# Optimization experiments

Hardware: AMD Instinct MI355X
Metric: run time of the kernel (lower is better)

Reference implementation:

```python
import jax, jax.numpy as jnp
import numpy as np

PATCH = 4   # patch_size
TOPK = 2    # top_k

B, H, W, C = 4, 128, 128, 256
FF, E = 1024, 4


def setup_inputs() -> dict:
    key = jax.random.key(0)
    k1, k2, k3, k4 = jax.random.split(key, 4)
    x = jax.random.normal(k1, (B, H, W, C), dtype=jnp.float32)
    Wg = jax.random.normal(k2, (E, C), dtype=jnp.float32) * 0.01   # router gate (std=0.01 init)
    lim1 = (6.0 / (C + FF)) ** 0.5                                  # xavier_uniform bounds
    W1 = jax.random.uniform(k3, (E, FF, C), minval=-lim1, maxval=lim1, dtype=jnp.float32)
    b1 = jnp.zeros((E, FF), dtype=jnp.float32)
    W2 = jax.random.uniform(k4, (E, C, FF), minval=-lim1, maxval=lim1, dtype=jnp.float32)
    b2 = jnp.zeros((E, C), dtype=jnp.float32)
    return {"x": x, "Wg": Wg, "W1": W1, "b1": b1, "W2": W2, "b2": b2}


def reference(x, Wg, W1, b1, W2, b2):
    Bs, Hs, Ws, Cs = x.shape
    Es = Wg.shape[0]
    ph = pw = PATCH
    nh, nw = Hs // ph, Ws // pw
    P = nh * nw
    # [B, nh, ph, nw, pw, C]
    xp = x.reshape(Bs, nh, ph, nw, pw, Cs)
    # --- router: per-patch avg pool + linear gate ---
    means = xp.mean(axis=(2, 4))                                  # [B, nh, nw, C]
    logits = jnp.einsum('bhwc,ec->bhwe', means, Wg).reshape(Bs, P, Es)
    probs = jax.nn.softmax(logits, axis=-1)
    w, idx = jax.lax.top_k(probs, TOPK)                           # [B, P, K]
    w = w / (w.sum(axis=-1, keepdims=True) + 1e-9)
    # dense combine weights per expert: [B, P, E]
    comb = (jax.nn.one_hot(idx, Es, dtype=w.dtype) * w[..., None]).sum(axis=-2)
    # --- expert dispatch/combine over patch tokens ---
    tokens = xp.transpose(0, 1, 3, 2, 4, 5).reshape(Bs, P, ph * pw, Cs)  # [B,P,T,C]
    out = jnp.zeros_like(tokens)
    for e in range(Es):  # small fixed expert set
        h = jax.nn.gelu(jnp.einsum('bptc,fc->bptf', tokens, W1[e]) + b1[e],
                        approximate=False)
        y = jnp.einsum('bptf,cf->bptc', h, W2[e]) + b2[e]
        out = out + comb[:, :, e, None, None] * y
    # reassemble patches -> [B, H, W, C]
    out = out.reshape(Bs, nh, nw, ph, pw, Cs).transpose(0, 1, 3, 2, 4, 5)
    return out.reshape(Bs, Hs, Ws, Cs)
```

## Files before the change

### kernel.cpp

```cpp
#include <hip/hip_runtime.h>
#include <hip/hip_bf16.h>
#include <cstdint>

#define NB 4
#define NH 128
#define NW 128
#define NC 256
#define NFF 1024
#define NE 4
#define NPATCH 4096
#define NPAIR 16
#define PPB 4
#define BM 64
#define FFC 128
#define NCHUNK_TOT 16

typedef __attribute__((ext_vector_type(8))) short short8;
typedef __attribute__((ext_vector_type(8))) unsigned short ushort8;
typedef __attribute__((ext_vector_type(4))) float f32x4;

__device__ __forceinline__ unsigned short f2b(float f) {
  union { float f; uint32_t u; } v; v.f = f;
  uint32_t u = v.u + 0x7FFFu + ((v.u >> 16) & 1u);
  return (unsigned short)(u >> 16);
}

__device__ __forceinline__ float gelu_f(float v) {
  float u = v * v;
  float t = __builtin_fmaf(u, 0.044715f, 1.0f) * v;
  float e = __builtin_amdgcn_exp2f(t * -2.3022083f);
  return v * __builtin_amdgcn_rcpf(1.0f + e);
}

__device__ __forceinline__ void bar_lgkm() {
  asm volatile("s_waitcnt lgkmcnt(0)" ::: "memory");
  __builtin_amdgcn_s_barrier();
}

__global__ __launch_bounds__(256) void convert_kernel(
    const float* __restrict__ W1, const float* __restrict__ W2,
    unsigned short* __restrict__ W1b, unsigned short* __restrict__ W2b,
    int* __restrict__ cnt, int n) {
  int i = blockIdx.x * blockDim.x + threadIdx.x;
  if (i < NPAIR) cnt[i] = 0;
  if (i < n) {
    W1b[i] = f2b(W1[i]);
    W2b[i] = f2b(W2[i]);
  }
}

__global__ __launch_bounds__(256) void router_kernel(
    const float* __restrict__ x, const float* __restrict__ Wg,
    int* __restrict__ cnt, int* __restrict__ plist, float2* __restrict__ wlist) {
  int p = blockIdx.x;
  int b = p >> 10, pi = p & 1023;
  int phi = pi >> 5, pwi = pi & 31;
  int c = threadIdx.x;

  const float* base = x + (((size_t)(b * NH + phi * 4) * NW) + pwi * 4) * NC + c;
  float s = 0.f;
#pragma unroll
  for (int i = 0; i < 4; i++)
#pragma unroll
    for (int j = 0; j < 4; j++)
      s += base[(i * NW + j) * NC];
  float mean = s * (1.f / 16.f);

  __shared__ float m_lds[NC];
  __shared__ double logit_lds[NE];
  m_lds[c] = mean;
  __syncthreads();

  int wid = c >> 6, lane = c & 63;
  {
    const float* wg = Wg + wid * NC;
    double acc = 0.0;
#pragma unroll
    for (int q = 0; q < 4; q++)
      acc += (double)m_lds[lane + q * 64] * (double)wg[lane + q * 64];
    for (int off = 32; off; off >>= 1) acc += __shfl_down(acc, off);
    if (lane == 0) logit_lds[wid] = acc;
  }
  __syncthreads();

  if (c == 0) {
    double l[NE], pp[NE];
    double mx = -1e300;
#pragma unroll
    for (int i = 0; i < NE; i++) { l[i] = logit_lds[i]; mx = fmax(mx, l[i]); }
    double sum = 0.0;
#pragma unroll
    for (int i = 0; i < NE; i++) { pp[i] = exp(l[i] - mx); sum += pp[i]; }
#pragma unroll
    for (int i = 0; i < NE; i++) pp[i] /= sum;
    int i1 = 0; double p1 = pp[0];
    for (int i = 1; i < NE; i++) if (pp[i] > p1) { p1 = pp[i]; i1 = i; }
    int i2 = -1; double p2 = -1.0;
    for (int i = 0; i < NE; i++) {
      if (i == i1) continue;
      if (pp[i] > p2) { p2 = pp[i]; i2 = i; }
    }
    double den = p1 + p2 + 1e-9;
    float w1 = (float)(p1 / den), w2 = (float)(p2 / den);
    int pr = i1 * NE + i2;
    int pos = atomicAdd(&cnt[pr], 1);
    plist[pr * NPATCH + pos] = p;
    wlist[pr * NPATCH + pos] = make_float2(w1, w2);
  }
}

__global__ __launch_bounds__(64) void worklist_kernel(
    const int* __restrict__ cnt, int* __restrict__ wl) {
  int lane = threadIdx.x;
  int cA[8], cB[8], mx = 0;
#pragma unroll
  for (int xc = 0; xc < 8; ++xc) {
    cA[xc] = (cnt[xc] + PPB - 1) / PPB;
    cB[xc] = (cnt[xc + 8] + PPB - 1) / PPB;
    int t = cA[xc] + cB[xc];
    mx = (t > mx) ? t : mx;
  }
  if (lane == 0) wl[0] = 8 * mx;
  int x = lane & 7, sub = lane >> 3;
  int nA = cA[x], tot = cA[x] + cB[x];
  for (int r = sub; r < mx; r += 8) {
    int ent = -1;
    if (r < nA) ent = (x << 12) | (r * PPB);
    else if (r < tot) ent = ((x + 8) << 12) | ((r - nA) * PPB);
    wl[1 + x + 8 * r] = ent;
  }
}

__global__ __launch_bounds__(512, 4) void ffn_kernel(
    const float* __restrict__ x, const float* __restrict__ b1,
    const float* __restrict__ b2, const unsigned short* __restrict__ W1b,
    const unsigned short* __restrict__ W2b, const int* __restrict__ cnt,
    const int* __restrict__ plist, const float2* __restrict__ wlist,
    const int* __restrict__ wl, float* __restrict__ out) {
  __shared__ unsigned short Xl[BM * NC];
  __shared__ unsigned short Hl[2][BM * FFC];

  int slot = blockIdx.x;
  if (slot >= wl[0]) return;
  int ent = wl[1 + slot];
  if (ent < 0) return;
  int pr = ent >> 12, pbase = ent & 4095;
  int e1 = pr >> 2, e2 = pr & 3;
  int n = cnt[pr];

  int tid = threadIdx.x, lane = tid & 63, wid = tid >> 6;
  int l15 = lane & 15;
  int kgrp = (lane >> 4) * 8;

  const int*    pl  = plist + pr * NPATCH + pbase;
  const float2* wlp = wlist + pr * NPATCH + pbase;

  float wvA[PPB], wvB[PPB];
#pragma unroll
  for (int q = 0; q < PPB; q++) {
    if (pbase + q < n) { float2 w = wlp[q]; wvA[q] = w.x; wvB[q] = w.y; }
    else { wvA[q] = 0.f; wvB[q] = 0.f; }
  }

  {
    int r  = tid >> 3;
    int c0 = (tid & 7) * 32;
    int pid = (pbase + (r >> 4) < n) ? pl[r >> 4] : -1;
    int t = r & 15;
    if (pid >= 0) {
      int b = pid >> 10, pi = pid & 1023;
      int phi = pi >> 5, pwi = pi & 31;
      const float* src =
          x + (((size_t)(b * NH + phi * 4 + (t >> 2)) * NW) + pwi * 4 + (t & 3)) * NC + c0;
#pragma unroll
      for (int q = 0; q < 4; q++) {
        float4 v0 = *reinterpret_cast<const float4*>(src + q * 8);
        float4 v1 = *reinterpret_cast<const float4*>(src + q * 8 + 4);
        ushort8 h;
        h[0] = f2b(v0.x); h[1] = f2b(v0.y); h[2] = f2b(v0.z); h[3] = f2b(v0.w);
        h[4] = f2b(v1.x); h[5] = f2b(v1.y); h[6] = f2b(v1.z); h[7] = f2b(v1.w);
        int boff = (r * 512 + (c0 + q * 8) * 2) ^ ((r & 7) << 4);
        *reinterpret_cast<ushort8*>((char*)Xl + boff) = h;
      }
    } else {
      ushort8 h = (ushort8)0;
#pragma unroll
      for (int q = 0; q < 4; q++) {
        int boff = (r * 512 + (c0 + q * 8) * 2) ^ ((r & 7) << 4);
        *reinterpret_cast<ushort8*>((char*)Xl + boff) = h;
      }
    }
  }
  bar_lgkm();

  if (wid < 4) {
    int wf = wid;
    const unsigned short* W1A = W1b + (size_t)e1 * NFF * NC;
    const unsigned short* W1B = W1b + (size_t)e2 * NFF * NC;
    const float* b1A = b1 + e1 * NFF;
    const float* b1B = b1 + e2 * NFF;

    f32x4 acc1[2][4];
    ushort4 hreg[8];

#pragma unroll 1
    for (int j = 0; j < NCHUNK_TOT; ++j) {
      const unsigned short* W1e = (j < 8) ? W1A : W1B;
      const float* b1e = (j < 8) ? b1A : b1B;
      int fc = j & 7;
#pragma unroll
      for (int a = 0; a < 2; a++)
#pragma unroll
        for (int b = 0; b < 4; b++)
#pragma unroll
          for (int q = 0; q < 4; q++) acc1[a][b][q] = 0.f;

#pragma unroll
      for (int ks = 0; ks < 8; ++ks) {
        int k = ks * 32 + kgrp;
        short8 bX[4];
#pragma unroll
        for (int nt = 0; nt < 4; nt++) {
          int row = nt * 16 + l15;
          int boff = (row * 512 + k * 2) ^ ((row & 7) << 4);
          bX[nt] = *reinterpret_cast<const short8*>((const char*)Xl + boff);
        }
        short8 aW[2];
#pragma unroll
        for (int ftl = 0; ftl < 2; ftl++) {
          int f = fc * FFC + wf * 32 + ftl * 16 + l15;
          aW[ftl] = *reinterpret_cast<const short8*>(W1e + (size_t)f * NC + k);
        }
        __builtin_amdgcn_s_setprio(1);
#pragma unroll
        for (int ftl = 0; ftl < 2; ftl++)
#pragma unroll
          for (int nt = 0; nt < 4; nt++)
            acc1[ftl][nt] = __builtin_amdgcn_mfma_f32_16x16x32_bf16(
                aW[ftl], bX[nt], acc1[ftl][nt], 0, 0, 0);
        __builtin_amdgcn_s_setprio(0);
      }

#pragma unroll
      for (int ftl = 0; ftl < 2; ftl++) {
        int f0 = wf * 32 + ftl * 16 + (lane >> 4) * 4;
        float4 bv = *reinterpret_cast<const float4*>(b1e + fc * FFC + f0);
#pragma unroll
        for (int nt = 0; nt < 4; nt++) {
          float w = (j < 8) ? wvA[nt] : wvB[nt];
          ushort4 hp;
          hp.x = f2b(gelu_f(acc1[ftl][nt][0] + bv.x) * w);
          hp.y = f2b(gelu_f(acc1[ftl][nt][1] + bv.y) * w);
          hp.z = f2b(gelu_f(acc1[ftl][nt][2] + bv.z) * w);
          hp.w = f2b(gelu_f(acc1[ftl][nt][3] + bv.w) * w);
          hreg[ftl * 4 + nt] = hp;
        }
      }
      unsigned short* Hb = &Hl[j & 1][0];
#pragma unroll
      for (int g = 0; g < 8; ++g) {
        int ftl = g >> 2, nt = g & 3;
        int token = nt * 16 + l15;
        int f0 = wf * 32 + ftl * 16 + (lane >> 4) * 4;
        int boff = (token * 256 + f0 * 2) ^ ((token & 7) << 4);
        *reinterpret_cast<ushort4*>((char*)Hb + boff) = hreg[g];
      }
      bar_lgkm();
    }
  } else {
    int wc = wid - 4;
    const unsigned short* W2A = W2b + (size_t)e1 * NC * NFF;
    const unsigned short* W2B = W2b + (size_t)e2 * NC * NFF;

    f32x4 acc2[4][4];
#pragma unroll
    for (int a = 0; a < 4; a++)
#pragma unroll
      for (int b = 0; b < 4; b++)
#pragma unroll
        for (int q = 0; q < 4; q++) acc2[a][b][q] = 0.f;

    bar_lgkm();

#pragma unroll 1
    for (int j = 0; j < NCHUNK_TOT; ++j) {
      const unsigned short* W2e = (j < 8) ? W2A : W2B;
      int fcp = j & 7;
      const unsigned short* Hb = &Hl[j & 1][0];
#pragma unroll
      for (int ks = 0; ks < 4; ++ks) {
        int kf = ks * 32 + kgrp;
        short8 aH[4];
#pragma unroll
        for (int rt = 0; rt < 4; rt++) {
          int row = rt * 16 + l15;
          int boff = (row * 256 + kf * 2) ^ ((row & 7) << 4);
          aH[rt] = *reinterpret_cast<const short8*>((const char*)Hb + boff);
        }
        short8 bW[4];
#pragma unroll
        for (int ct = 0; ct < 4; ct++) {
          int c = wc * 64 + ct * 16 + l15;
          bW[ct] = *reinterpret_cast<const short8*>(
              W2e + (size_t)c * NFF + fcp * FFC + kf);
        }
        __builtin_amdgcn_s_setprio(1);
#pragma unroll
        for (int ct = 0; ct < 4; ct++)
#pragma unroll
          for (int rt = 0; rt < 4; rt++)
            acc2[ct][rt] = __builtin_amdgcn_mfma_f32_16x16x32_bf16(
                aH[rt], bW[ct], acc2[ct][rt], 0, 0, 0);
        __builtin_amdgcn_s_setprio(0);
      }
      if (j < NCHUNK_TOT - 1) bar_lgkm();
    }

    float b2A4[4], b2B4[4];
#pragma unroll
    for (int ct = 0; ct < 4; ct++) {
      int c = wc * 64 + ct * 16 + l15;
      b2A4[ct] = b2[e1 * NC + c];
      b2B4[ct] = b2[e2 * NC + c];
    }
#pragma unroll
    for (int rt = 0; rt < 4; rt++) {
      if (pbase + rt >= n) continue;
      int pid = pl[rt];
      float wA = wvA[rt], wB = wvB[rt];
      int b = pid >> 10, pi = pid & 1023;
      int phi = pi >> 5, pwi = pi & 31;
#pragma unroll
      for (int i2 = 0; i2 < 4; i2++) {
        int t = (lane >> 4) * 4 + i2;
        float* dst =
            out + (((size_t)(b * NH + phi * 4 + (t >> 2)) * NW) + pwi * 4 + (t & 3)) * NC;
#pragma unroll
        for (int ct = 0; ct < 4; ct++) {
          int c = wc * 64 + ct * 16 + l15;
          dst[c] = acc2[ct][rt][i2] + wA * b2A4[ct] + wB * b2B4[ct];
        }
      }
    }
  }
}

extern "C" void kernel_launch(void* const* d_in, const int* in_sizes, int n_in,
                              void* d_out, int out_size, void* d_ws, size_t ws_size,
                              hipStream_t stream) {
  const float* x  = (const float*)d_in[0];
  const float* Wg = (const float*)d_in[1];
  const float* W1 = (const float*)d_in[2];
  const float* b1 = (const float*)d_in[3];
  const float* W2 = (const float*)d_in[4];
  const float* b2 = (const float*)d_in[5];
  float* out = (float*)d_out;

  char* ws = (char*)d_ws;
  unsigned short* W1b = (unsigned short*)ws;
  unsigned short* W2b = (unsigned short*)(ws + (size_t)2 * 1024 * 1024);
  int*    cnt   = (int*)(ws + (size_t)4 * 1024 * 1024);
  int*    plist = (int*)(ws + (size_t)4 * 1024 * 1024 + 256);
  float2* wlist = (float2*)(ws + (size_t)4 * 1024 * 1024 + 256 +
                            (size_t)NPAIR * NPATCH * sizeof(int));
  int*    wl    = (int*)(ws + (size_t)5 * 1024 * 1024);

  convert_kernel<<<dim3(4096), dim3(256), 0, stream>>>(W1, W2, W1b, W2b, cnt, NE * NFF * NC);
  router_kernel<<<dim3(NPATCH), dim3(256), 0, stream>>>(x, Wg, cnt, plist, wlist);
  worklist_kernel<<<dim3(1), dim3(64), 0, stream>>>(cnt, wl);

  ffn_kernel<<<dim3(8208), dim3(512), 0, stream>>>(
      x, b1, b2, W1b, W2b, cnt, plist, wlist, wl, out);
}
```

Before: 438.2 us.

## Stream FFN weight tiles into per-wave LDS ring via async global_load_lds

W1 and W2 weight fragments now go through a 3-slot per-wave LDS ring filled with global_load_lds, issued two steps ahead and gated with vmcnt waits, instead of being loaded straight from global memory into registers. b1 biases are staged once in LDS, and H is stored to LDS directly rather than buffered in registers. The aim is to hide weight-load latency behind MFMA work. In exchange, LDS use grows a lot and launch bounds drop to 2 blocks, which reduces occupancy and adds a risk of a read-versus-overwrite race when ring slots are reused.

```diff
diff --git a/kernel.cpp b/kernel.cpp
--- a/kernel.cpp
+++ b/kernel.cpp
@@ -14,6 +14,7 @@
 #define BM 64
 #define FFC 128
 #define NCHUNK_TOT 16
+#define RING 3
 
 typedef __attribute__((ext_vector_type(8))) short short8;
 typedef __attribute__((ext_vector_type(8))) unsigned short ushort8;
@@ -35,6 +36,12 @@
 __device__ __forceinline__ void bar_lgkm() {
   asm volatile("s_waitcnt lgkmcnt(0)" ::: "memory");
   __builtin_amdgcn_s_barrier();
+}
+
+__device__ __forceinline__ void gload_lds16(const void* g, void* l) {
+  __builtin_amdgcn_global_load_lds(
+      (const __attribute__((address_space(1))) unsigned int*)g,
+      (__attribute__((address_space(3))) unsigned int*)l, 16, 0, 0);
 }
 
 __global__ __launch_bounds__(256) void convert_kernel(
@@ -131,7 +138,7 @@
   }
 }
 
-__global__ __launch_bounds__(512, 4) void ffn_kernel(
+__global__ __launch_bounds__(512, 2) void ffn_kernel(
     const float* __restrict__ x, const float* __restrict__ b1,
     const float* __restrict__ b2, const unsigned short* __restrict__ W1b,
     const unsigned short* __restrict__ W2b, const int* __restrict__ cnt,
@@ -139,10 +146,13 @@
     const int* __restrict__ wl, float* __restrict__ out) {
   __shared__ unsigned short Xl[BM * NC];
   __shared__ unsigned short Hl[2][BM * FFC];
-
-  int slot = blockIdx.x;
-  if (slot >= wl[0]) return;
-  int ent = wl[1 + slot];
+  __shared__ unsigned short W1r[4][RING][1024];
+  __shared__ unsigned short W2r[4][RING][2048];
+  __shared__ float b1lds[2 * NFF];
+
+  int slotb = blockIdx.x;
+  if (slotb >= wl[0]) return;
+  int ent = wl[1 + slotb];
   if (ent < 0) return;
   int pr = ent >> 12, pbase = ent & 4095;
   int e1 = pr >> 2, e2 = pr & 3;
@@ -150,7 +160,7 @@
 
   int tid = threadIdx.x, lane = tid & 63, wid = tid >> 6;
   int l15 = lane & 15;
-  int kgrp = (lane >> 4) * 8;
+  int kgl = lane >> 4;
 
   const int*    pl  = plist + pr * NPATCH + pbase;
   const float2* wlp = wlist + pr * NPATCH + pbase;
@@ -160,6 +170,12 @@
   for (int q = 0; q < PPB; q++) {
     if (pbase + q < n) { float2 w = wlp[q]; wvA[q] = w.x; wvB[q] = w.y; }
     else { wvA[q] = 0.f; wvB[q] = 0.f; }
+  }
+
+  {
+    int o = tid * 4;
+    const float* sp = (o < NFF) ? (b1 + e1 * NFF + o) : (b1 + e2 * NFF + (o - NFF));
+    *reinterpret_cast<float4*>(&b1lds[o]) = *reinterpret_cast<const float4*>(sp);
   }
 
   {
@@ -191,22 +207,39 @@
       }
     }
   }
-  bar_lgkm();
+
+  asm volatile("s_waitcnt vmcnt(0)" ::: "memory");
+
+  const unsigned short* W1A = W1b + (size_t)e1 * NFF * NC;
+  const unsigned short* W1B = W1b + (size_t)e2 * NFF * NC;
+  const unsigned short* W2A = W2b + (size_t)e1 * NC * NFF;
+  const unsigned short* W2B = W2b + (size_t)e2 * NC * NFF;
 
   if (wid < 4) {
     int wf = wid;
-    const unsigned short* W1A = W1b + (size_t)e1 * NFF * NC;
-    const unsigned short* W1B = W1b + (size_t)e2 * NFF * NC;
-    const float* b1A = b1 + e1 * NFF;
-    const float* b1B = b1 + e2 * NFF;
+
+    auto g1_issue = [&](int s) {
+      s = (s > 127) ? 127 : s;
+      int jj = s >> 3, kk = s & 7;
+      const unsigned short* W1e = (jj < 8) ? W1A : W1B;
+      int f0 = (jj & 7) * FFC + wf * 32;
+      int k0 = kk * 32;
+      int sl = s % 3;
+#pragma unroll
+      for (int q = 0; q < 2; q++) {
+        const unsigned short* src =
+            W1e + (size_t)(f0 + (lane & 31)) * NC + k0 + (q * 2 + (lane >> 5)) * 8;
+        gload_lds16(src, (void*)&W1r[wf][sl][q * 512]);
+      }
+    };
+
+    g1_issue(0);
+    g1_issue(1);
+    bar_lgkm();
 
     f32x4 acc1[2][4];
-    ushort4 hreg[8];
-
 #pragma unroll 1
     for (int j = 0; j < NCHUNK_TOT; ++j) {
-      const unsigned short* W1e = (j < 8) ? W1A : W1B;
-      const float* b1e = (j < 8) ? b1A : b1B;
       int fc = j & 7;
 #pragma unroll
       for (int a = 0; a < 2; a++)
@@ -217,7 +250,16 @@
 
 #pragma unroll
       for (int ks = 0; ks < 8; ++ks) {
-        int k = ks * 32 + kgrp;
+        int s = j * 8 + ks;
+        g1_issue(s + 2);
+        int sl = s % 3;
+        asm volatile("s_waitcnt vmcnt(4)" ::: "memory");
+        short8 aW[2];
+#pragma unroll
+        for (int ftl = 0; ftl < 2; ftl++)
+          aW[ftl] = *reinterpret_cast<const short8*>(
+              &W1r[wf][sl][kgl * 256 + (ftl * 16 + l15) * 8]);
+        int k = ks * 32 + kgl * 8;
         short8 bX[4];
 #pragma unroll
         for (int nt = 0; nt < 4; nt++) {
@@ -225,12 +267,6 @@
           int boff = (row * 512 + k * 2) ^ ((row & 7) << 4);
           bX[nt] = *reinterpret_cast<const short8*>((const char*)Xl + boff);
         }
-        short8 aW[2];
-#pragma unroll
-        for (int ftl = 0; ftl < 2; ftl++) {
-          int f = fc * FFC + wf * 32 + ftl * 16 + l15;
-          aW[ftl] = *reinterpret_cast<const short8*>(W1e + (size_t)f * NC + k);
-        }
         __builtin_amdgcn_s_setprio(1);
 #pragma unroll
         for (int ftl = 0; ftl < 2; ftl++)
@@ -241,10 +277,12 @@
         __builtin_amdgcn_s_setprio(0);
       }
 
+      unsigned short* Hb = &Hl[j & 1][0];
+      int sideOff = (j < 8) ? 0 : NFF;
 #pragma unroll
       for (int ftl = 0; ftl < 2; ftl++) {
         int f0 = wf * 32 + ftl * 16 + (lane >> 4) * 4;
-        float4 bv = *reinterpret_cast<const float4*>(b1e + fc * FFC + f0);
+        float4 bv = *reinterpret_cast<const float4*>(&b1lds[sideOff + fc * FFC + f0]);
 #pragma unroll
         for (int nt = 0; nt < 4; nt++) {
           float w = (j < 8) ? wvA[nt] : wvB[nt];
@@ -253,24 +291,32 @@
           hp.y = f2b(gelu_f(acc1[ftl][nt][1] + bv.y) * w);
           hp.z = f2b(gelu_f(acc1[ftl][nt][2] + bv.z) * w);
           hp.w = f2b(gelu_f(acc1[ftl][nt][3] + bv.w) * w);
-          hreg[ftl * 4 + nt] = hp;
+          int token = nt * 16 + l15;
+          int boff = (token * 256 + f0 * 2) ^ ((token & 7) << 4);
+          *reinterpret_cast<ushort4*>((char*)Hb + boff) = hp;
         }
-      }
-      unsigned short* Hb = &Hl[j & 1][0];
-#pragma unroll
-      for (int g = 0; g < 8; ++g) {
-        int ftl = g >> 2, nt = g & 3;
-        int token = nt * 16 + l15;
-        int f0 = wf * 32 + ftl * 16 + (lane >> 4) * 4;
-        int boff = (token * 256 + f0 * 2) ^ ((token & 7) << 4);
-        *reinterpret_cast<ushort4*>((char*)Hb + boff) = hreg[g];
       }
       bar_lgkm();
     }
   } else {
     int wc = wid - 4;
-    const unsigned short* W2A = W2b + (size_t)e1 * NC * NFF;
-    const unsigned short* W2B = W2b + (size_t)e2 * NC * NFF;
+    int c0g = wc * 64;
+
+    auto g2_issue = [&](int s) {
+      s = (s > 63) ? 63 : s;
+      int jj = s >> 2, kk = s & 3;
+      const unsigned short* W2e = (jj < 8) ? W2A : W2B;
+      int k0 = (jj & 7) * FFC + kk * 32;
+      int sl = s % 3;
+      const unsigned short* srow = W2e + (size_t)(c0g + lane) * NFF + k0;
+#pragma unroll
+      for (int q = 0; q < 4; q++)
+        gload_lds16(srow + q * 8, (void*)&W2r[wc][sl][q * 512]);
+    };
+
+    g2_issue(0);
+    g2_issue(1);
+    bar_lgkm();
 
     f32x4 acc2[4][4];
 #pragma unroll
@@ -284,12 +330,14 @@
 
 #pragma unroll 1
     for (int j = 0; j < NCHUNK_TOT; ++j) {
-      const unsigned short* W2e = (j < 8) ? W2A : W2B;
-      int fcp = j & 7;
       const unsigned short* Hb = &Hl[j & 1][0];
 #pragma unroll
       for (int ks = 0; ks < 4; ++ks) {
-        int kf = ks * 32 + kgrp;
+        int s = j * 4 + ks;
+        g2_issue(s + 2);
+        int sl = s % 3;
+        asm volatile("s_waitcnt vmcnt(8)" ::: "memory");
+        int kf = ks * 32 + kgl * 8;
         short8 aH[4];
 #pragma unroll
         for (int rt = 0; rt < 4; rt++) {
@@ -299,11 +347,9 @@
         }
         short8 bW[4];
 #pragma unroll
-        for (int ct = 0; ct < 4; ct++) {
-          int c = wc * 64 + ct * 16 + l15;
+        for (int ct = 0; ct < 4; ct++)
           bW[ct] = *reinterpret_cast<const short8*>(
-              W2e + (size_t)c * NFF + fcp * FFC + kf);
-        }
+              &W2r[wc][sl][kgl * 512 + (ct * 16 + l15) * 8]);
         __builtin_amdgcn_s_setprio(1);
 #pragma unroll
         for (int ct = 0; ct < 4; ct++)
```

After: 617.0 us. 40.8% more time.

## Enlarge FFN tiles to six patches with 32x32 MFMA and async LDS weight staging

Applied to the files above, without the earlier changes.

Raises the per-block tile from 4 to 6 patches (96 tokens) and switches both GEMMs to 32x32x16 bf16 MFMA with fragment-ordered LDS layouts for X and H. Weight tiles are now streamed into double-buffered LDS with global_load_lds, so the direct per-wave global weight loads go away. b1 is staged in LDS, and the W2 consumer waves run one chunk behind the W1 producer waves over a single H buffer. The aim is more weight reuse per block and overlap of weight fetch with MFMA work. In exchange, occupancy drops to 2 blocks per CU and each chunk now needs two barriers.

```diff
diff --git a/kernel.cpp b/kernel.cpp
--- a/kernel.cpp
+++ b/kernel.cpp
@@ -10,14 +10,14 @@
 #define NE 4
 #define NPATCH 4096
 #define NPAIR 16
-#define PPB 4
-#define BM 64
+#define PPB 6
+#define BM 96
 #define FFC 128
 #define NCHUNK_TOT 16
 
 typedef __attribute__((ext_vector_type(8))) short short8;
 typedef __attribute__((ext_vector_type(8))) unsigned short ushort8;
-typedef __attribute__((ext_vector_type(4))) float f32x4;
+typedef __attribute__((ext_vector_type(16))) float f32x16;
 
 __device__ __forceinline__ unsigned short f2b(float f) {
   union { float f; uint32_t u; } v; v.f = f;
@@ -35,6 +35,12 @@
 __device__ __forceinline__ void bar_lgkm() {
   asm volatile("s_waitcnt lgkmcnt(0)" ::: "memory");
   __builtin_amdgcn_s_barrier();
+}
+
+__device__ __forceinline__ void gload_lds16(const void* g, void* l) {
+  __builtin_amdgcn_global_load_lds(
+      (const __attribute__((address_space(1))) unsigned int*)g,
+      (__attribute__((address_space(3))) unsigned int*)l, 16, 0, 0);
 }
 
 __global__ __launch_bounds__(256) void convert_kernel(
@@ -131,26 +137,28 @@
   }
 }
 
-__global__ __launch_bounds__(512, 4) void ffn_kernel(
+__global__ __launch_bounds__(512, 2) void ffn_kernel(
     const float* __restrict__ x, const float* __restrict__ b1,
     const float* __restrict__ b2, const unsigned short* __restrict__ W1b,
     const unsigned short* __restrict__ W2b, const int* __restrict__ cnt,
     const int* __restrict__ plist, const float2* __restrict__ wlist,
     const int* __restrict__ wl, float* __restrict__ out) {
-  __shared__ unsigned short Xl[BM * NC];
-  __shared__ unsigned short Hl[2][BM * FFC];
-
-  int slot = blockIdx.x;
-  if (slot >= wl[0]) return;
-  int ent = wl[1 + slot];
+  __shared__ unsigned short Xf[3 * 16 * 512];
+  __shared__ unsigned short Hf[3 * 8 * 512];
+  __shared__ unsigned short W1r[4][2][4 * 512];
+  __shared__ unsigned short W2r[4][2][4 * 512];
+  __shared__ float b1l[2 * NFF];
+
+  int slotb = blockIdx.x;
+  if (slotb >= wl[0]) return;
+  int ent = wl[1 + slotb];
   if (ent < 0) return;
   int pr = ent >> 12, pbase = ent & 4095;
   int e1 = pr >> 2, e2 = pr & 3;
   int n = cnt[pr];
 
   int tid = threadIdx.x, lane = tid & 63, wid = tid >> 6;
-  int l15 = lane & 15;
-  int kgrp = (lane >> 4) * 8;
+  int l31 = lane & 31, lh = lane >> 5;
 
   const int*    pl  = plist + pr * NPATCH + pbase;
   const float2* wlp = wlist + pr * NPATCH + pbase;
@@ -162,183 +170,211 @@
     else { wvA[q] = 0.f; wvB[q] = 0.f; }
   }
 
-  {
-    int r  = tid >> 3;
-    int c0 = (tid & 7) * 32;
+  if (tid < 384) {
+    int r  = tid >> 2;
+    int c0 = (tid & 3) * 64;
     int pid = (pbase + (r >> 4) < n) ? pl[r >> 4] : -1;
     int t = r & 15;
+    int tt = r >> 5, t32 = r & 31;
     if (pid >= 0) {
       int b = pid >> 10, pi = pid & 1023;
       int phi = pi >> 5, pwi = pi & 31;
       const float* src =
           x + (((size_t)(b * NH + phi * 4 + (t >> 2)) * NW) + pwi * 4 + (t & 3)) * NC + c0;
 #pragma unroll
-      for (int q = 0; q < 4; q++) {
-        float4 v0 = *reinterpret_cast<const float4*>(src + q * 8);
-        float4 v1 = *reinterpret_cast<const float4*>(src + q * 8 + 4);
+      for (int kb = 0; kb < 8; kb++) {
+        float4 v0 = *reinterpret_cast<const float4*>(src + kb * 8);
+        float4 v1 = *reinterpret_cast<const float4*>(src + kb * 8 + 4);
         ushort8 h;
         h[0] = f2b(v0.x); h[1] = f2b(v0.y); h[2] = f2b(v0.z); h[3] = f2b(v0.w);
         h[4] = f2b(v1.x); h[5] = f2b(v1.y); h[6] = f2b(v1.z); h[7] = f2b(v1.w);
-        int boff = (r * 512 + (c0 + q * 8) * 2) ^ ((r & 7) << 4);
-        *reinterpret_cast<ushort8*>((char*)Xl + boff) = h;
+        int k = c0 + kb * 8;
+        int uidx = (tt * 16 + (k >> 4)) * 512 + (((k >> 3) & 1) * 32 + t32) * 8;
+        *reinterpret_cast<ushort8*>(&Xf[uidx]) = h;
       }
     } else {
       ushort8 h = (ushort8)0;
 #pragma unroll
-      for (int q = 0; q < 4; q++) {
-        int boff = (r * 512 + (c0 + q * 8) * 2) ^ ((r & 7) << 4);
-        *reinterpret_cast<ushort8*>((char*)Xl + boff) = h;
-      }
-    }
-  }
-  bar_lgkm();
+      for (int kb = 0; kb < 8; kb++) {
+        int k = c0 + kb * 8;
+        int uidx = (tt * 16 + (k >> 4)) * 512 + (((k >> 3) & 1) * 32 + t32) * 8;
+        *reinterpret_cast<ushort8*>(&Xf[uidx]) = h;
+      }
+    }
+  } else {
+    int o = (tid - 384) * 16;
+#pragma unroll
+    for (int q = 0; q < 4; q++) {
+      int idx = o + q * 4;
+      const float* sp = (idx < NFF) ? (b1 + e1 * NFF + idx) : (b1 + e2 * NFF + (idx - NFF));
+      *reinterpret_cast<float4*>(&b1l[idx]) = *reinterpret_cast<const float4*>(sp);
+    }
+  }
+
+  asm volatile("s_waitcnt vmcnt(0)" ::: "memory");
+
+  const unsigned short* W1A = W1b + (size_t)e1 * NFF * NC;
+  const unsigned short* W1B = W1b + (size_t)e2 * NFF * NC;
+  const unsigned short* W2A = W2b + (size_t)e1 * NC * NFF;
+  const unsigned short* W2B = W2b + (size_t)e2 * NC * NFF;
 
   if (wid < 4) {
     int wf = wid;
-    const unsigned short* W1A = W1b + (size_t)e1 * NFF * NC;
-    const unsigned short* W1B = W1b + (size_t)e2 * NFF * NC;
-    const float* b1A = b1 + e1 * NFF;
-    const float* b1B = b1 + e2 * NFF;
-
-    f32x4 acc1[2][4];
-    ushort4 hreg[8];
+    auto g1_issue = [&](int g) {
+      g = (g > 63) ? 63 : g;
+      int jj = g >> 2, st = g & 3;
+      const unsigned short* W1e = (jj < 8) ? W1A : W1B;
+      int fg = (jj & 7) * FFC + wf * 32 + l31;
+      int slot = g & 1;
+#pragma unroll
+      for (int q = 0; q < 4; q++) {
+        const unsigned short* src = W1e + (size_t)fg * NC + st * 64 + q * 16 + lh * 8;
+        gload_lds16(src, (void*)&W1r[wf][slot][q * 512]);
+      }
+    };
+
+    g1_issue(0);
+    bar_lgkm();
+
+    f32x16 acc0, acc1v, acc2v;
+    ushort4 hreg[12];
 
 #pragma unroll 1
     for (int j = 0; j < NCHUNK_TOT; ++j) {
-      const unsigned short* W1e = (j < 8) ? W1A : W1B;
-      const float* b1e = (j < 8) ? b1A : b1B;
       int fc = j & 7;
-#pragma unroll
-      for (int a = 0; a < 2; a++)
-#pragma unroll
-        for (int b = 0; b < 4; b++)
-#pragma unroll
-          for (int q = 0; q < 4; q++) acc1[a][b][q] = 0.f;
-
-#pragma unroll
-      for (int ks = 0; ks < 8; ++ks) {
-        int k = ks * 32 + kgrp;
-        short8 bX[4];
-#pragma unroll
-        for (int nt = 0; nt < 4; nt++) {
-          int row = nt * 16 + l15;
-          int boff = (row * 512 + k * 2) ^ ((row & 7) << 4);
-          bX[nt] = *reinterpret_cast<const short8*>((const char*)Xl + boff);
+      int sideOff = (j < 8) ? 0 : NFF;
+      acc0 = (f32x16)0.f; acc1v = (f32x16)0.f; acc2v = (f32x16)0.f;
+
+#pragma unroll
+      for (int s = 0; s < 4; ++s) {
+        g1_issue(j * 4 + s + 1);
+        asm volatile("s_waitcnt vmcnt(4)" ::: "memory");
+        int slot = s & 1;
+#pragma unroll
+        for (int kq = 0; kq < 4; ++kq) {
+          int kk = s * 4 + kq;
+          short8 aW = *reinterpret_cast<const short8*>(&W1r[wf][slot][kq * 512 + lane * 8]);
+          short8 bX0 = *reinterpret_cast<const short8*>(&Xf[(0 * 16 + kk) * 512 + lane * 8]);
+          short8 bX1 = *reinterpret_cast<const short8*>(&Xf[(1 * 16 + kk) * 512 + lane * 8]);
+          short8 bX2 = *reinterpret_cast<const short8*>(&Xf[(2 * 16 + kk) * 512 + lane * 8]);
+          acc0  = __builtin_amdgcn_mfma_f32_32x32x16_bf16(aW, bX0, acc0, 0, 0, 0);
+          acc1v = __builtin_amdgcn_mfma_f32_32x32x16_bf16(aW, bX1, acc1v, 0, 0, 0);
+          acc2v = __builtin_amdgcn_mfma_f32_32x32x16_bf16(aW, bX2, acc2v, 0, 0, 0);
         }
-        short8 aW[2];
-#pragma unroll
-        for (int ftl = 0; ftl < 2; ftl++) {
-          int f = fc * FFC + wf * 32 + ftl * 16 + l15;
-          aW[ftl] = *reinterpret_cast<const short8*>(W1e + (size_t)f * NC + k);
+      }
+
+#pragma unroll
+      for (int tt = 0; tt < 3; ++tt) {
+        const f32x16& A = (tt == 0) ? acc0 : (tt == 1) ? acc1v : acc2v;
+        float wlo = (j < 8) ? wvA[tt * 2]     : wvB[tt * 2];
+        float whi = (j < 8) ? wvA[tt * 2 + 1] : wvB[tt * 2 + 1];
+        float w = (l31 >= 16) ? whi : wlo;
+#pragma unroll
+        for (int q = 0; q < 4; ++q) {
+          int qs = q * 8 + lh * 4;
+          float4 bv = *reinterpret_cast<const float4*>(&b1l[sideOff + fc * FFC + wf * 32 + qs]);
+          ushort4 hp;
+          hp.x = f2b(gelu_f(A[q * 4 + 0] + bv.x) * w);
+          hp.y = f2b(gelu_f(A[q * 4 + 1] + bv.y) * w);
+          hp.z = f2b(gelu_f(A[q * 4 + 2] + bv.z) * w);
+          hp.w = f2b(gelu_f(A[q * 4 + 3] + bv.w) * w);
+          hreg[tt * 4 + q] = hp;
         }
-        __builtin_amdgcn_s_setprio(1);
-#pragma unroll
-        for (int ftl = 0; ftl < 2; ftl++)
-#pragma unroll
-          for (int nt = 0; nt < 4; nt++)
-            acc1[ftl][nt] = __builtin_amdgcn_mfma_f32_16x16x32_bf16(
-                aW[ftl], bX[nt], acc1[ftl][nt], 0, 0, 0);
-        __builtin_amdgcn_s_setprio(0);
-      }
-
-#pragma unroll
-      for (int ftl = 0; ftl < 2; ftl++) {
-        int f0 = wf * 32 + ftl * 16 + (lane >> 4) * 4;
-        float4 bv = *reinterpret_cast<const float4*>(b1e + fc * FFC + f0);
-#pragma unroll
-        for (int nt = 0; nt < 4; nt++) {
-          float w = (j < 8) ? wvA[nt] : wvB[nt];
-          ushort4 hp;
-          hp.x = f2b(gelu_f(acc1[ftl][nt][0] + bv.x) * w);
-          hp.y = f2b(gelu_f(acc1[ftl][nt][1] + bv.y) * w);
-          hp.z = f2b(gelu_f(acc1[ftl][nt][2] + bv.z) * w);
-          hp.w = f2b(gelu_f(acc1[ftl][nt][3] + bv.w) * w);
-          hreg[ftl * 4 + nt] = hp;
+      }
+      bar_lgkm();
+#pragma unroll
+      for (int tt = 0; tt < 3; ++tt) {
+#pragma unroll
+        for (int q = 0; q < 4; ++q) {
+          int qs = q * 8 + lh * 4;
+          int page = tt * 8 + wf * 2 + (qs >> 4);
+          int uidx = page * 512 + (((qs >> 3) & 1) * 32 + l31) * 8 + (qs & 4);
+          *reinterpret_cast<ushort4*>(&Hf[uidx]) = hreg[tt * 4 + q];
         }
-      }
-      unsigned short* Hb = &Hl[j & 1][0];
-#pragma unroll
-      for (int g = 0; g < 8; ++g) {
-        int ftl = g >> 2, nt = g & 3;
-        int token = nt * 16 + l15;
-        int f0 = wf * 32 + ftl * 16 + (lane >> 4) * 4;
-        int boff = (token * 256 + f0 * 2) ^ ((token & 7) << 4);
-        *reinterpret_cast<ushort4*>((char*)Hb + boff) = hreg[g];
       }
       bar_lgkm();
     }
   } else {
     int wc = wid - 4;
-    const unsigned short* W2A = W2b + (size_t)e1 * NC * NFF;
-    const unsigned short* W2B = W2b + (size_t)e2 * NC * NFF;
-
-    f32x4 acc2[4][4];
-#pragma unroll
-    for (int a = 0; a < 4; a++)
-#pragma unroll
-      for (int b = 0; b < 4; b++)
-#pragma unroll
-        for (int q = 0; q < 4; q++) acc2[a][b][q] = 0.f;
-
+    auto g2_issue = [&](int g) {
+      g = (g > 63) ? 63 : g;
+      int jj = g >> 2, st = g & 3;
+      const unsigned short* W2e = (jj < 8) ? W2A : W2B;
+      int fcn = jj & 7;
+      int slot = g & 1;
+#pragma unroll
+      for (int q = 0; q < 4; q++) {
+        int ct = q >> 1, kkis = q & 1;
+        const unsigned short* src = W2e +
+            (size_t)(wc * 64 + ct * 32 + l31) * NFF +
+            fcn * FFC + st * 32 + kkis * 16 + lh * 8;
+        gload_lds16(src, (void*)&W2r[wc][slot][q * 512]);
+      }
+    };
+
+    g2_issue(0);
     bar_lgkm();
+
+    f32x16 y00 = (f32x16)0.f, y01 = (f32x16)0.f, y02 = (f32x16)0.f;
+    f32x16 y10 = (f32x16)0.f, y11 = (f32x16)0.f, y12 = (f32x16)0.f;
+
+    auto consume = [&](int jc) {
+#pragma unroll
+      for (int s = 0; s < 4; ++s) {
+        g2_issue(jc * 4 + s + 1);
+        asm volatile("s_waitcnt vmcnt(4)" ::: "memory");
+        int slot = s & 1;
+#pragma unroll
+        for (int kkis = 0; kkis < 2; ++kkis) {
+          int kkf = s * 2 + kkis;
+          short8 aH0 = *reinterpret_cast<const short8*>(&Hf[(0 * 8 + kkf) * 512 + lane * 8]);
+          short8 aH1 = *reinterpret_cast<const short8*>(&Hf[(1 * 8 + kkf) * 512 + lane * 8]);
+          short8 aH2 = *reinterpret_cast<const short8*>(&Hf[(2 * 8 + kkf) * 512 + lane * 8]);
+          short8 bW0 = *reinterpret_cast<const short8*>(&W2r[wc][slot][(0 * 2 + kkis) * 512 + lane * 8]);
+          short8 bW1 = *reinterpret_cast<const short8*>(&W2r[wc][slot][(1 * 2 + kkis) * 512 + lane * 8]);
+          y00 = __builtin_amdgcn_mfma_f32_32x32x16_bf16(aH0, bW0, y00, 0, 0, 0);
+          y01 = __builtin_amdgcn_mfma_f32_32x32x16_bf16(aH1, bW0, y01, 0, 0, 0);
+          y02 = __builtin_amdgcn_mfma_f32_32x32x16_bf16(aH2, bW0, y02, 0, 0, 0);
+          y10 = __builtin_amdgcn_mfma_f32_32x32x16_bf16(aH0, bW1, y10, 0, 0, 0);
+          y11 = __builtin_amdgcn_mfma_f32_32x32x16_bf16(aH1, bW1, y11, 0, 0, 0);
+          y12 = __builtin_amdgcn_mfma_f32_32x32x16_bf16(aH2, bW1, y12, 0, 0, 0);
+        }
+      }
+    };
 
 #pragma unroll 1
     for (int j = 0; j < NCHUNK_TOT; ++j) {
-      const unsigned short* W2e = (j < 8) ? W2A : W2B;
-      int fcp = j & 7;
-      const unsigned short* Hb = &Hl[j & 1][0];
-#pragma unroll
-      for (int ks = 0; ks < 4; ++ks) {
-        int kf = ks * 32 + kgrp;
-        short8 aH[4];
-#pragma unroll
-        for (int rt = 0; rt < 4; rt++) {
-          int row = rt * 16 + l15;
-          int boff = (row * 256 + kf * 2) ^ ((row & 7) << 4);
-          aH[rt] = *reinterpret_cast<const short8*>((const char*)Hb + boff);
-        }
-        short8 bW[4];
-#pragma unroll
-        for (int ct = 0; ct < 4; ct++) {
-          int c = wc * 64 + ct * 16 + l15;
-          bW[ct] = *reinterpret_cast<const short8*>(
-              W2e + (size_t)c * NFF + fcp * FFC + kf);
-        }
-        __builtin_amdgcn_s_setprio(1);
-#pragma unroll
-        for (int ct = 0; ct < 4; ct++)
-#pragma unroll
-          for (int rt = 0; rt < 4; rt++)
-            acc2[ct][rt] = __builtin_amdgcn_mfma_f32_16x16x32_bf16(
-                aH[rt], bW[ct], acc2[ct][rt], 0, 0, 0);
-        __builtin_amdgcn_s_setprio(0);
-      }
-      if (j < NCHUNK_TOT - 1) bar_lgkm();
-    }
-
-    float b2A4[4], b2B4[4];
-#pragma unroll
-    for (int ct = 0; ct < 4; ct++) {
-      int c = wc * 64 + ct * 16 + l15;
-      b2A4[ct] = b2[e1 * NC + c];
-      b2B4[ct] = b2[e2 * NC + c];
-    }
-#pragma unroll
-    for (int rt = 0; rt < 4; rt++) {
-      if (pbase + rt >= n) continue;
-      int pid = pl[rt];
-      float wA = wvA[rt], wB = wvB[rt];
-      int b = pid >> 10, pi = pid & 1023;
-      int phi = pi >> 5, pwi = pi & 31;
-#pragma unroll
-      for (int i2 = 0; i2 < 4; i2++) {
-        int t = (lane >> 4) * 4 + i2;
-        float* dst =
-            out + (((size_t)(b * NH + phi * 4 + (t >> 2)) * NW) + pwi * 4 + (t & 3)) * NC;
-#pragma unroll
-        for (int ct = 0; ct < 4; ct++) {
-          int c = wc * 64 + ct * 16 + l15;
-          dst[c] = acc2[ct][rt][i2] + wA * b2A4[ct] + wB * b2B4[ct];
+      if (j > 0) consume(j - 1);
+      bar_lgkm();
+      bar_lgkm();
+    }
+    consume(NCHUNK_TOT - 1);
+
+#pragma unroll
+    for (int ct = 0; ct < 2; ++ct) {
+      int cc = wc * 64 + ct * 32 + l31;
+      float bA = b2[e1 * NC + cc];
+      float bB = b2[e2 * NC + cc];
+#pragma unroll
+      for (int tt = 0; tt < 3; ++tt) {
+        const f32x16& Y = (ct == 0) ? ((tt == 0) ? y00 : (tt == 1) ? y01 : y02)
+                                    : ((tt == 0) ? y10 : (tt == 1) ? y11 : y12);
+#pragma unroll
+        for (int q = 0; q < 4; ++q) {
+          int pslot = tt * 2 + (q >> 1);
+          if (pbase + pslot >= n) continue;
+          int pid = pl[pslot];
+          float wA = wvA[pslot], wB = wvB[pslot];
+          int b = pid >> 10, pi = pid & 1023;
+          int phi = pi >> 5, pwi = pi & 31;
+          float bias = wA * bA + wB * bB;
+#pragma unroll
+          for (int i = 0; i < 4; ++i) {
+            int tok = 8 * (q & 1) + 4 * lh + i;
+            float* dst =
+                out + (((size_t)(b * NH + phi * 4 + (tok >> 2)) * NW) + pwi * 4 + (tok & 3)) * NC;
+            dst[cc] = Y[q * 4 + i] + bias;
+          }
         }
       }
     }
@@ -369,6 +405,6 @@
   router_kernel<<<dim3(NPATCH), dim3(256), 0, stream>>>(x, Wg, cnt, plist, wlist);
   worklist_kernel<<<dim3(1), dim3(64), 0, stream>>>(cnt, wl);
 
-  ffn_kernel<<<dim3(8208), dim3(512), 0, stream>>>(
+  ffn_kernel<<<dim3(5472), dim3(512), 0, stream>>>(
       x, b1, b2, W1b, W2b, cnt, plist, wlist, wl, out);
 }
```

After: 490.1 us. 1.12x slower.
